# Optimization experiments

Measured on AMD Instinct MI355X. Metric: run time of the kernel, lower is better.

The kernel has to match this reference:

```python
import jax, jax.numpy as jnp
import numpy as np

EDGE_TYPES = 7
TIME_STEP = 5
STATE_DIM = 1024


def setup_inputs() -> dict:
    key = jax.random.key(0)
    ks = jax.random.split(key, 8)
    B, T, N, DF = 4, 15, 15, 25600
    S, E = STATE_DIM, EDGE_TYPES
    # weights ~ N(0, 0.01), biases zero, matching _initialization()
    return {
        "pose_features": jax.random.normal(ks[0], (B, T, N, DF), jnp.float32),
        "W_compress": jax.random.normal(ks[1], (DF, S), jnp.float32) * 0.01,
        "b_compress": jnp.zeros((S,), jnp.float32),
        "W_edge": jax.random.normal(ks[2], (E, S, S), jnp.float32) * 0.01,
        "b_edge": jnp.zeros((E, S), jnp.float32),
        "W_att": jax.random.normal(ks[3], (E, 2 * S), jnp.float32) * 0.01,
        "b_att": jnp.zeros((E,), jnp.float32),
        "W_r": jax.random.normal(ks[4], (2 * S, S), jnp.float32) * 0.01,
        "b_r": jnp.zeros((S,), jnp.float32),
        "W_z": jax.random.normal(ks[5], (2 * S, S), jnp.float32) * 0.01,
        "b_z": jnp.zeros((S,), jnp.float32),
        "W_h": jax.random.normal(ks[6], (2 * S, S), jnp.float32) * 0.01,
        "b_h": jnp.zeros((S,), jnp.float32),
    }


def reference(pose_features, W_compress, b_compress, W_edge, b_edge,
              W_att, b_att, W_r, b_r, W_z, b_z, W_h, b_h):
    B, T, N, DF = pose_features.shape
    S = W_compress.shape[1]
    E = W_edge.shape[0]
    x = pose_features.reshape(B * T, N, DF)
    prop = x @ W_compress + b_compress                      # [M, N, S]
    # attention Linear over concat(row, col) == row-part + col-part (rank-1 broadcast,
    # avoids materializing the [M, N, N, 2S] repeat/cat tensor; identical math)
    Wa_row, Wa_col = W_att[:, :S], W_att[:, S:]
    scores = None
    for _ in range(1 + TIME_STEP):
        msg = jnp.einsum('bnd,edh->benh', prop, W_edge) + b_edge[None, :, None, :]  # [M,E,N,S]
        row = jnp.einsum('bend,ed->ben', msg, Wa_row)       # [M, E, N]
        col = jnp.einsum('bend,ed->ben', msg, Wa_col)
        scores = jax.nn.sigmoid(row[..., :, None] + col[..., None, :]
                                + b_att[None, :, None, None])   # [M, E, N, N]
        merged = jnp.einsum('beij,bejd->bid', scores, msg)  # [M, N, S]
        a = jnp.concatenate([merged, prop], axis=-1)        # [M, N, 2S]
        r = jax.nn.sigmoid(a @ W_r + b_r)
        z = jax.nn.sigmoid(a @ W_z + b_z)
        h_hat = jnp.tanh(jnp.concatenate([merged, r * prop], axis=-1) @ W_h + b_h)
        prop = (1 - z) * prop + z * h_hat
    box_states = scores.transpose(0, 2, 3, 1)               # [M, N, N, E]
    action_score = ((1 - box_states[..., 0:1]) * box_states).sum(axis=2)
    action_score = action_score.reshape(B, T, N, E)
    actor_score = (1 - box_states[..., 0]).reshape(B, T, N, N)
    acty_score = jax.nn.softmax(
        (action_score * actor_score.sum(axis=-1)[..., None]).sum(axis=2)[:, :, 1:],
        axis=-1)
    return action_score, acty_score, actor_score
```

## Files before the change

kernel.cpp:

```cpp
#include <hip/hip_runtime.h>
#include <hip/hip_bf16.h>

typedef unsigned short bf16_t;
typedef __bf16 bf16x8 __attribute__((ext_vector_type(8)));
typedef float f32x4 __attribute__((ext_vector_type(4)));
typedef unsigned short ushort8_t __attribute__((ext_vector_type(8)));

__device__ __forceinline__ unsigned short f2bf(float x){
  union { __hip_bfloat16 h; unsigned short u; } c;
  c.h = __float2bfloat16(x);
  return c.u;
}
__device__ __forceinline__ float bf2f(bf16_t u){
  union { unsigned short u; __hip_bfloat16 h; } c;
  c.u = u;
  return __bfloat162float(c.h);
}
__device__ __forceinline__ ushort8_t cvt8(float4 a, float4 b){
  ushort8_t r;
  r[0]=f2bf(a.x); r[1]=f2bf(a.y); r[2]=f2bf(a.z); r[3]=f2bf(a.w);
  r[4]=f2bf(b.x); r[5]=f2bf(b.y); r[6]=f2bf(b.z); r[7]=f2bf(b.w);
  return r;
}

__device__ __forceinline__ size_t pidx(int m, int k, int KT){
  const int r = m & 127, c = (k >> 3) & 3;
  const int cs = c ^ ((r >> 1) & 3);
  return ((size_t)((m >> 7)*KT + (k >> 5)))*4096 + r*32 + cs*8 + (k & 7);
}

template<int MODE>
__global__ __launch_bounds__(512, 4)
void gemm256(const void* __restrict__ Aptr, int KTA ,
             const bf16_t* __restrict__ Bpk, int KTB,
             float* __restrict__ C, int ldc, size_t csplit,
             int M, int KchunkT)
{
  __shared__ __align__(16) bf16_t As[2][8192];
  __shared__ __align__(16) bf16_t Bs[2][4096];
  const int tid = threadIdx.x;
  const int w = tid >> 6, lane = tid & 63;
  const int wm = w >> 1, wn = w & 1;
  const int lr = lane & 15, kq = lane >> 4;
  int bcol, brow, bks;
  if (MODE == 0)      { bcol = blockIdx.x; brow = blockIdx.y; bks = blockIdx.z; }
  else if (MODE == 1) { bks = blockIdx.x;  bcol = blockIdx.y; brow = blockIdx.z; }
  else { brow = blockIdx.x & 3; bks = blockIdx.z*2 + (blockIdx.x >> 2); bcol = blockIdx.y; }
  const int gn0 = bcol*128;
  const int kt0 = bks*KchunkT, nt = KchunkT;

  const int aoff = (w & 3)*1024 + lane*8;
  const int asub = w >> 2;
  ushort8_t va0, va1, vb0;
  const bf16_t* Bg = Bpk + ((size_t)bcol*KTB + kt0)*4096 + w*512 + lane*8;
  const bf16_t* Ag = nullptr;
  const float *Af0 = nullptr, *Af1 = nullptr;
  if (MODE == 2) {
    const int r  = aoff >> 5;
    const int cs = (aoff >> 3) & 3;
    const int c  = cs ^ ((r >> 1) & 3);
    const int g0 = min(brow*256 + asub*128 + r,      M-1);
    const int g1 = min(brow*256 + asub*128 + r + 16, M-1);
    Af0 = (const float*)Aptr + (size_t)g0*KTA + (size_t)kt0*32 + c*8;
    Af1 = (const float*)Aptr + (size_t)g1*KTA + (size_t)kt0*32 + c*8;
  } else {
    Ag = (const bf16_t*)Aptr + ((size_t)(2*brow + asub)*KTA + kt0)*4096 + aoff;
  }
  bf16_t* Al = &As[0][0] + asub*4096 + aoff;
  bf16_t* Bl = &Bs[0][0] + w*512 + lane*8;

#define LDT(t) do { \
    if (MODE == 2) { \
      const float* a0 = Af0 + (size_t)(t)*32; \
      const float* a1 = Af1 + (size_t)(t)*32; \
      va0 = cvt8(*(const float4*)a0, *(const float4*)(a0 + 4)); \
      va1 = cvt8(*(const float4*)a1, *(const float4*)(a1 + 4)); \
    } else { \
      va0 = *(const ushort8_t*)(Ag + (size_t)(t)*4096); \
      va1 = *(const ushort8_t*)(Ag + (size_t)(t)*4096 + 512); \
    } \
    vb0 = *(const ushort8_t*)(Bg + (size_t)(t)*4096); \
  } while(0)
#define WRT(b) do { \
    *(ushort8_t*)(Al + (b)*8192) = va0; \
    *(ushort8_t*)(Al + (b)*8192 + 512) = va1; \
    *(ushort8_t*)(Bl + (b)*4096) = vb0; } while(0)

  LDT(0); WRT(0);
  if (nt > 1) LDT(1);
  asm volatile("s_waitcnt lgkmcnt(0)" ::: "memory");
  __builtin_amdgcn_s_barrier();
  __builtin_amdgcn_sched_barrier(0);

  const int kqs = kq ^ ((lr >> 1) & 3);
  const int abase = (wm >> 1)*4096 + ((wm & 1)*64 + lr)*32 + kqs*8;
  const int bbase = (wn*64 + lr)*32 + kqs*8;
  f32x4 acc[4][4] = {};

  for (int t = 0; t < nt; ++t) {
    const int cb = t & 1;
    const bf16_t* Ab = &As[0][0] + cb*8192 + abase;
    const bf16_t* Bb = &Bs[0][0] + cb*4096 + bbase;
    bf16x8 af[4], bfr[4];
#pragma unroll
    for (int mi = 0; mi < 4; mi++) af[mi]  = *(const bf16x8*)(Ab + mi*512);
#pragma unroll
    for (int ni = 0; ni < 4; ni++) bfr[ni] = *(const bf16x8*)(Bb + ni*512);
    if (t + 1 < nt) WRT(cb ^ 1);
    if (t + 2 < nt) LDT(t + 2);
    __builtin_amdgcn_s_setprio(1);
#pragma unroll
    for (int mi = 0; mi < 4; mi++)
#pragma unroll
      for (int ni = 0; ni < 4; ni++)
        acc[mi][ni] = __builtin_amdgcn_mfma_f32_16x16x32_bf16(af[mi], bfr[ni], acc[mi][ni], 0, 0, 0);
    __builtin_amdgcn_s_setprio(0);
    asm volatile("s_waitcnt lgkmcnt(0)" ::: "memory");
    __builtin_amdgcn_s_barrier();
    __builtin_amdgcn_sched_barrier(0);
  }
#undef LDT
#undef WRT

#pragma unroll
  for (int mi = 0; mi < 4; mi++) {
#pragma unroll
    for (int ni = 0; ni < 4; ni++) {
      const int col = gn0 + wn*64 + ni*16 + lr;
#pragma unroll
      for (int i = 0; i < 4; i++) {
        const int row = brow*256 + wm*64 + mi*16 + kq*4 + i;
        if (row < M)
          C[(size_t)bks*csplit + (size_t)row*ldc + col] = acc[mi][ni][i];
      }
    }
  }
}

__global__ void pack_b(const float* __restrict__ src, bf16_t* __restrict__ dst,
                       int srcldN, int KT, int n0t)
{
  const int ntb = blockIdx.x, kt = blockIdx.y;
  __shared__ float s[32][132];
  for (int i = threadIdx.x; i < 4096; i += 256) {
    const int kl = i >> 7, nl = i & 127;
    s[kl][nl] = src[(size_t)(kt*32 + kl)*srcldN + ntb*128 + nl];
  }
  __syncthreads();
  bf16_t* dt = dst + ((size_t)(n0t + ntb)*KT + kt)*4096;
  for (int u = threadIdx.x; u < 512; u += 256) {
    const int r = u >> 2, c = u & 3;
    const int cs = c ^ ((r >> 1) & 3);
    *(ushort4*)(dt + r*32 + cs*8) =
      make_ushort4(f2bf(s[c*8+0][r]), f2bf(s[c*8+1][r]), f2bf(s[c*8+2][r]), f2bf(s[c*8+3][r]));
    *(ushort4*)(dt + r*32 + cs*8 + 4) =
      make_ushort4(f2bf(s[c*8+4][r]), f2bf(s[c*8+5][r]), f2bf(s[c*8+6][r]), f2bf(s[c*8+7][r]));
  }
}

__global__ void reduce_compress(const float* __restrict__ part, const float* __restrict__ bias,
                                float* __restrict__ prop, bf16_t* __restrict__ Xp)
{
  const int idx = blockIdx.x*256 + threadIdx.x;
  const int m = idx >> 10, d = idx & 1023;
  float v = bias[d];
#pragma unroll
  for (int z = 0; z < 8; z++) v += part[(size_t)z*921600 + idx];
  prop[idx] = v;
  Xp[pidx(m, 1024 + d, 64)] = f2bf(v);
}

__global__ void reduce_merged(const float* __restrict__ part, const float* __restrict__ rowsumS,
                              const float* __restrict__ be,
                              bf16_t* __restrict__ Xp, bf16_t* __restrict__ Xhp)
{
  const int idx = blockIdx.x*256 + threadIdx.x;
  const int m = idx >> 10, d = idx & 1023;
  const int b = m/15, i = m - b*15;
  float v = 0.f;
#pragma unroll
  for (int z = 0; z < 8; z++) v += part[(size_t)z*921600 + idx];
#pragma unroll
  for (int e = 0; e < 7; e++)
    v += rowsumS[(b*7 + e)*15 + i] * be[e*1024 + d];
  const bf16_t o = f2bf(v);
  Xp [pidx(m, d, 64)] = o;
  Xhp[pidx(m, d, 64)] = o;
}

__global__ void reduce_rz(const float* __restrict__ part, const float* __restrict__ bias,
                          const float* __restrict__ prop, float* __restrict__ Zbuf,
                          bf16_t* __restrict__ Xhp)
{
  const int idx = blockIdx.x*256 + threadIdx.x;
  const int m = idx >> 11, c = idx & 2047;
  float v = bias[c];
#pragma unroll
  for (int z = 0; z < 4; z++) v += part[(size_t)z*1843200 + idx];
  v = 1.f / (1.f + __expf(-v));
  if (c < 1024) Xhp[pidx(m, 1024 + c, 64)] = f2bf(v * prop[(size_t)m*1024 + c]);
  else          Zbuf[(size_t)m*1024 + (c - 1024)] = v;
}

__global__ void reduce_h(const float* __restrict__ part, const float* __restrict__ bias,
                         const float* __restrict__ Zbuf, float* __restrict__ prop,
                         bf16_t* __restrict__ Xp)
{
  const int idx = blockIdx.x*256 + threadIdx.x;
  const int m = idx >> 10, d = idx & 1023;
  float v = bias[d];
#pragma unroll
  for (int z = 0; z < 4; z++) v += part[(size_t)z*921600 + idx];
  v = tanhf(v);
  const float zz = Zbuf[idx];
  const float pn = (1.f - zz)*prop[idx] + zz*v;
  prop[idx] = pn;
  Xp[pidx(m, 1024 + d, 64)] = f2bf(pn);
}

__global__ void compute_u(const float* __restrict__ We, const float* __restrict__ Wa,
                          float* __restrict__ u_row, float* __restrict__ u_col)
{
  const int w = threadIdx.x >> 6, lane = threadIdx.x & 63;
  const int idx = blockIdx.x*4 + w;
  const int e = idx >> 10, h = idx & 1023;
  const float* wep = We + ((size_t)e*1024 + h)*1024;
  const float* wr  = Wa + (size_t)e*2048;
  const float* wc  = wr + 1024;
  float ar = 0.f, ac = 0.f;
#pragma unroll
  for (int t = 0; t < 16; t++) {
    const float v = wep[lane + 64*t];
    ar += v*wr[lane + 64*t];
    ac += v*wc[lane + 64*t];
  }
  for (int off = 32; off; off >>= 1) { ar += __shfl_down(ar, off); ac += __shfl_down(ac, off); }
  if (lane == 0) { u_row[idx] = ar; u_col[idx] = ac; }
}

__global__ void crc_kernel(const float* __restrict__ be, const float* __restrict__ Wa,
                           float* __restrict__ crc)
{
  const int w = threadIdx.x >> 6, lane = threadIdx.x & 63;
  for (int idx = w; idx < 14; idx += 4) {
    const int e = idx >> 1, which = idx & 1;
    const float* bp = be + e*1024;
    const float* wp = Wa + (size_t)e*2048 + which*1024;
    float a = 0.f;
#pragma unroll
    for (int t = 0; t < 16; t++) a += bp[lane + 64*t]*wp[lane + 64*t];
    for (int off = 32; off; off >>= 1) a += __shfl_down(a, off);
    if (lane == 0) crc[which*7 + e] = a;
  }
}

__global__ void attn_kernel(const float* __restrict__ prop, const float* __restrict__ u_row,
                            const float* __restrict__ u_col, const float* __restrict__ crc,
                            const float* __restrict__ b_att, float* __restrict__ scores,
                            float* __restrict__ rowsumS)
{
  const int b = blockIdx.x, e = blockIdx.y;
  __shared__ float rowv[15], colv[15], sc_s[225];
  const int w = threadIdx.x >> 6, lane = threadIdx.x & 63;
  const float* ur = u_row + (size_t)e*1024;
  const float* uc = u_col + (size_t)e*1024;
  for (int n = w; n < 15; n += 4) {
    const float* pr = prop + (size_t)(b*15 + n)*1024;
    float ar = 0.f, ac = 0.f;
#pragma unroll
    for (int t = 0; t < 16; t++) {
      const float pv = pr[lane + 64*t];
      ar += pv*ur[lane + 64*t];
      ac += pv*uc[lane + 64*t];
    }
    for (int off = 32; off; off >>= 1) { ar += __shfl_down(ar, off); ac += __shfl_down(ac, off); }
    if (lane == 0) { rowv[n] = ar; colv[n] = ac; }
  }
  __syncthreads();
  const float base = b_att[e] + crc[e] + crc[7 + e];
  for (int idx = threadIdx.x; idx < 225; idx += 256) {
    const int i = idx/15, j = idx - i*15;
    const float s = 1.f / (1.f + __expf(-(rowv[i] + colv[j] + base)));
    scores[((size_t)(b*7 + e)*15 + i)*15 + j] = s;
    sc_s[idx] = s;
  }
  __syncthreads();
  if (threadIdx.x < 15) {
    float rs = 0.f;
#pragma unroll
    for (int j = 0; j < 15; j++) rs += sc_s[threadIdx.x*15 + j];
    rowsumS[(b*7 + e)*15 + threadIdx.x] = rs;
  }
}

__global__ __launch_bounds__(512)
void qmix_kernel(const float* __restrict__ prop, const float* __restrict__ scores,
                 bf16_t* __restrict__ Qp)
{
  const int b = blockIdx.x;
  const int d = blockIdx.y*512 + threadIdx.x;
  __shared__ float ss[1575];
  for (int idx = threadIdx.x; idx < 1575; idx += 512)
    ss[idx] = scores[(size_t)b*1575 + idx];
  float pv[15];
#pragma unroll
  for (int j = 0; j < 15; j++)
    pv[j] = prop[(size_t)(b*15 + j)*1024 + d];
  __syncthreads();
  for (int e = 0; e < 7; e++)
#pragma unroll
    for (int i = 0; i < 15; i++) {
      const float* se = ss + (e*15 + i)*15;
      float a = 0.f;
#pragma unroll
      for (int j = 0; j < 15; j++) a += se[j]*pv[j];
      Qp[pidx(b*15 + i, e*1024 + d, 224)] = f2bf(a);
    }
}

__global__ void cat2_kernel(const float* __restrict__ a, const float* __restrict__ b,
                            float* __restrict__ o)
{
  const int i = blockIdx.x*256 + threadIdx.x;
  if (i < 1024) o[i] = a[i];
  else if (i < 2048) o[i] = b[i - 1024];
}

__global__ void finalize_kernel(const float* __restrict__ scores, float* __restrict__ out)
{
  const int b = blockIdx.x;
  __shared__ float sc[1575];
  __shared__ float act[105];
  __shared__ float asum[15];
  __shared__ float t2[7];
  for (int idx = threadIdx.x; idx < 1575; idx += 256)
    sc[idx] = scores[(size_t)b*1575 + idx];
  __syncthreads();
  for (int idx = threadIdx.x; idx < 105; idx += 256) {
    const int i = idx/7, e = idx - i*7;
    float a = 0.f;
#pragma unroll
    for (int j = 0; j < 15; j++)
      a += (1.f - sc[i*15 + j]) * sc[(e*15 + i)*15 + j];
    act[idx] = a;
    out[(size_t)b*105 + idx] = a;
  }
  for (int idx = threadIdx.x; idx < 225; idx += 256) {
    const int i = idx/15, j = idx - i*15;
    out[6660 + (size_t)b*225 + idx] = 1.f - sc[i*15 + j];
  }
  if (threadIdx.x < 15) {
    const int i = threadIdx.x;
    float s = 0.f;
#pragma unroll
    for (int j = 0; j < 15; j++) s += 1.f - sc[i*15 + j];
    asum[i] = s;
  }
  __syncthreads();
  if (threadIdx.x < 7) {
    const int e = threadIdx.x;
    float t = 0.f;
#pragma unroll
    for (int i = 0; i < 15; i++) t += act[i*7 + e]*asum[i];
    t2[e] = t;
  }
  __syncthreads();
  if (threadIdx.x == 0) {
    float mx = -1e30f;
    for (int e = 1; e < 7; e++) mx = fmaxf(mx, t2[e]);
    float s = 0.f, ex[6];
    for (int e = 1; e < 7; e++) { ex[e-1] = __expf(t2[e] - mx); s += ex[e-1]; }
    for (int e = 1; e < 7; e++) out[6300 + (size_t)b*6 + (e-1)] = ex[e-1]/s;
  }
}

extern "C" void kernel_launch(void* const* d_in, const int* in_sizes, int n_in,
                              void* d_out, int out_size, void* d_ws, size_t ws_size,
                              hipStream_t stream)
{
  const float* pose = (const float*)d_in[0];
  const float* Wc   = (const float*)d_in[1];
  const float* bc   = (const float*)d_in[2];
  const float* We   = (const float*)d_in[3];
  const float* be   = (const float*)d_in[4];
  const float* Wa   = (const float*)d_in[5];
  const float* ba   = (const float*)d_in[6];
  const float* Wr   = (const float*)d_in[7];
  const float* br   = (const float*)d_in[8];
  const float* Wz   = (const float*)d_in[9];
  const float* bz   = (const float*)d_in[10];
  const float* Wh   = (const float*)d_in[11];
  const float* bh   = (const float*)d_in[12];
  float* out = (float*)d_out;

  char* p = (char*)d_ws;
  auto alloc = [&](size_t b) { char* r = p; p += (b + 255) & ~(size_t)255; return r; };
  bf16_t* Wstackp = (bf16_t*)alloc(8ull*224*8192);
  bf16_t* Wrzp    = (bf16_t*)alloc(16ull*64*8192);
  bf16_t* Whp     = (bf16_t*)alloc(8ull*64*8192);
  bf16_t* Xp      = (bf16_t*)alloc(8ull*64*8192);
  bf16_t* Xhp     = (bf16_t*)alloc(8ull*64*8192);
  float*  prop    = (float*) alloc(900ull*1024*4);
  float*  scores  = (float*) alloc(60ull*1575*4);
  float*  rowsumS = (float*) alloc(60ull*105*4);
  float*  u_row   = (float*) alloc(7168*4);
  float*  u_col   = (float*) alloc(7168*4);
  float*  crc     = (float*) alloc(64);
  float*  brzv    = (float*) alloc(2048*4);
  char* r1 = alloc(134400000ull);
  bf16_t* Wcp     = (bf16_t*)r1;
  bf16_t* Qp      = (bf16_t*)r1;
  float*  Zbuf    = (float*) (r1 + 14680064ull);
  float*  partbuf = (float*) (r1 + 52428800ull);

  compute_u<<<1792, 256, 0, stream>>>(We, Wa, u_row, u_col);
  crc_kernel<<<1, 256, 0, stream>>>(be, Wa, crc);
  cat2_kernel<<<8, 256, 0, stream>>>(br, bz, brzv);
  pack_b<<<dim3(8,800), 256, 0, stream>>>(Wc, Wcp, 1024, 800, 0);
  pack_b<<<dim3(8,224), 256, 0, stream>>>(We, Wstackp, 1024, 224, 0);
  pack_b<<<dim3(8,64),  256, 0, stream>>>(Wr, Wrzp, 1024, 64, 0);
  pack_b<<<dim3(8,64),  256, 0, stream>>>(Wz, Wrzp, 1024, 64, 8);
  pack_b<<<dim3(8,64),  256, 0, stream>>>(Wh, Whp, 1024, 64, 0);

  gemm256<2><<<dim3(8,8,4), 512, 0, stream>>>(pose, 25600, Wcp, 800,
      partbuf, 1024, 921600ull, 900, 100);
  reduce_compress<<<3600, 256, 0, stream>>>(partbuf, bc, prop, Xp);

  for (int it = 0; it < 6; it++) {
    attn_kernel<<<dim3(60,7), 256, 0, stream>>>(prop, u_row, u_col, crc, ba,
                                                scores, rowsumS);
    if (it == 5) break;
    qmix_kernel<<<dim3(60,2), 512, 0, stream>>>(prop, scores, Qp);
    gemm256<1><<<dim3(8,8,4), 512, 0, stream>>>(Qp, 224, Wstackp, 224,
        partbuf, 1024, 921600ull, 900, 28);
    reduce_merged<<<3600, 256, 0, stream>>>(partbuf, rowsumS, be, Xp, Xhp);
    gemm256<0><<<dim3(16,4,4), 512, 0, stream>>>(Xp, 64, Wrzp, 64,
        partbuf, 2048, 1843200ull, 900, 16);
    reduce_rz<<<7200, 256, 0, stream>>>(partbuf, brzv, prop, Zbuf, Xhp);
    gemm256<0><<<dim3(8,4,4), 512, 0, stream>>>(Xhp, 64, Whp, 64,
        partbuf, 1024, 921600ull, 900, 16);
    reduce_h<<<3600, 256, 0, stream>>>(partbuf, bh, Zbuf, prop, Xp);
  }

  finalize_kernel<<<60, 256, 0, stream>>>(scores, out);
}
```

Before: 778.9 us.

## Fuse attention with qmix, double split-K on GEMMs, use nontemporal partial traffic

Attention scoring and the score-weighted mixing (qmix) are merged into one kernel per batch. It stages prop as bf16 in shared memory and computes all 7 edge types per block. Every GEMM now uses twice as many split-K chunks and more blocks, and the reduce kernels sum correspondingly more partials. Partial-buffer loads and stores, plus the fp32 pose loads, become nontemporal to avoid cache pollution. The intent is better CU occupancy and fewer launches, at the cost of more partial-sum traffic and slight extra bf16 rounding of prop in qmix.

```diff
diff --git a/kernel.cpp b/kernel.cpp
--- a/kernel.cpp
+++ b/kernel.cpp
@@ -16,10 +16,10 @@
   c.u = u;
   return __bfloat162float(c.h);
 }
-__device__ __forceinline__ ushort8_t cvt8(float4 a, float4 b){
+__device__ __forceinline__ ushort8_t cvt8v(f32x4 a, f32x4 b){
   ushort8_t r;
-  r[0]=f2bf(a.x); r[1]=f2bf(a.y); r[2]=f2bf(a.z); r[3]=f2bf(a.w);
-  r[4]=f2bf(b.x); r[5]=f2bf(b.y); r[6]=f2bf(b.z); r[7]=f2bf(b.w);
+  r[0]=f2bf(a[0]); r[1]=f2bf(a[1]); r[2]=f2bf(a[2]); r[3]=f2bf(a[3]);
+  r[4]=f2bf(b[0]); r[5]=f2bf(b[1]); r[6]=f2bf(b[2]); r[7]=f2bf(b[3]);
   return r;
 }
 
@@ -43,8 +43,7 @@
   const int wm = w >> 1, wn = w & 1;
   const int lr = lane & 15, kq = lane >> 4;
   int bcol, brow, bks;
-  if (MODE == 0)      { bcol = blockIdx.x; brow = blockIdx.y; bks = blockIdx.z; }
-  else if (MODE == 1) { bks = blockIdx.x;  bcol = blockIdx.y; brow = blockIdx.z; }
+  if (MODE == 1) { bks = blockIdx.x;  bcol = blockIdx.y; brow = blockIdx.z; }
   else { brow = blockIdx.x & 3; bks = blockIdx.z*2 + (blockIdx.x >> 2); bcol = blockIdx.y; }
   const int gn0 = bcol*128;
   const int kt0 = bks*KchunkT, nt = KchunkT;
@@ -73,8 +72,10 @@
     if (MODE == 2) { \
       const float* a0 = Af0 + (size_t)(t)*32; \
       const float* a1 = Af1 + (size_t)(t)*32; \
-      va0 = cvt8(*(const float4*)a0, *(const float4*)(a0 + 4)); \
-      va1 = cvt8(*(const float4*)a1, *(const float4*)(a1 + 4)); \
+      va0 = cvt8v(__builtin_nontemporal_load((const f32x4*)a0), \
+                  __builtin_nontemporal_load((const f32x4*)(a0 + 4))); \
+      va1 = cvt8v(__builtin_nontemporal_load((const f32x4*)a1), \
+                  __builtin_nontemporal_load((const f32x4*)(a1 + 4))); \
     } else { \
       va0 = *(const ushort8_t*)(Ag + (size_t)(t)*4096); \
       va1 = *(const ushort8_t*)(Ag + (size_t)(t)*4096 + 512); \
@@ -131,7 +132,8 @@
       for (int i = 0; i < 4; i++) {
         const int row = brow*256 + wm*64 + mi*16 + kq*4 + i;
         if (row < M)
-          C[(size_t)bks*csplit + (size_t)row*ldc + col] = acc[mi][ni][i];
+          __builtin_nontemporal_store(acc[mi][ni][i],
+              &C[(size_t)bks*csplit + (size_t)row*ldc + col]);
       }
     }
   }
@@ -165,7 +167,7 @@
   const int m = idx >> 10, d = idx & 1023;
   float v = bias[d];
 #pragma unroll
-  for (int z = 0; z < 8; z++) v += part[(size_t)z*921600 + idx];
+  for (int z = 0; z < 16; z++) v += __builtin_nontemporal_load(&part[(size_t)z*921600 + idx]);
   prop[idx] = v;
   Xp[pidx(m, 1024 + d, 64)] = f2bf(v);
 }
@@ -179,7 +181,7 @@
   const int b = m/15, i = m - b*15;
   float v = 0.f;
 #pragma unroll
-  for (int z = 0; z < 8; z++) v += part[(size_t)z*921600 + idx];
+  for (int z = 0; z < 16; z++) v += __builtin_nontemporal_load(&part[(size_t)z*921600 + idx]);
 #pragma unroll
   for (int e = 0; e < 7; e++)
     v += rowsumS[(b*7 + e)*15 + i] * be[e*1024 + d];
@@ -196,7 +198,7 @@
   const int m = idx >> 11, c = idx & 2047;
   float v = bias[c];
 #pragma unroll
-  for (int z = 0; z < 4; z++) v += part[(size_t)z*1843200 + idx];
+  for (int z = 0; z < 8; z++) v += __builtin_nontemporal_load(&part[(size_t)z*1843200 + idx]);
   v = 1.f / (1.f + __expf(-v));
   if (c < 1024) Xhp[pidx(m, 1024 + c, 64)] = f2bf(v * prop[(size_t)m*1024 + c]);
   else          Zbuf[(size_t)m*1024 + (c - 1024)] = v;
@@ -210,7 +212,7 @@
   const int m = idx >> 10, d = idx & 1023;
   float v = bias[d];
 #pragma unroll
-  for (int z = 0; z < 4; z++) v += part[(size_t)z*921600 + idx];
+  for (int z = 0; z < 8; z++) v += __builtin_nontemporal_load(&part[(size_t)z*921600 + idx]);
   v = tanhf(v);
   const float zz = Zbuf[idx];
   const float pn = (1.f - zz)*prop[idx] + zz*v;
@@ -254,18 +256,28 @@
   }
 }
 
-__global__ void attn_kernel(const float* __restrict__ prop, const float* __restrict__ u_row,
-                            const float* __restrict__ u_col, const float* __restrict__ crc,
-                            const float* __restrict__ b_att, float* __restrict__ scores,
-                            float* __restrict__ rowsumS)
-{
-  const int b = blockIdx.x, e = blockIdx.y;
-  __shared__ float rowv[15], colv[15], sc_s[225];
-  const int w = threadIdx.x >> 6, lane = threadIdx.x & 63;
-  const float* ur = u_row + (size_t)e*1024;
-  const float* uc = u_col + (size_t)e*1024;
-  for (int n = w; n < 15; n += 4) {
+template<int QM>
+__global__ __launch_bounds__(512)
+void attn_qmix(const float* __restrict__ prop, const float* __restrict__ u_row,
+               const float* __restrict__ u_col, const float* __restrict__ crc,
+               const float* __restrict__ b_att, float* __restrict__ scores,
+               float* __restrict__ rowsumS, bf16_t* __restrict__ Qp)
+{
+  const int b = blockIdx.x;
+  __shared__ bf16_t ps[15*1024];
+  __shared__ float ss[1575];
+  __shared__ float rv[105], cv[105];
+  const int tid = threadIdx.x;
+  const int w = tid >> 6, lane = tid & 63;
+
+  for (int idx = tid; idx < 15360; idx += 512)
+    ps[idx] = f2bf(prop[(size_t)b*15360 + idx]);
+
+  for (int p = w; p < 105; p += 8) {
+    const int e = p/15, n = p - e*15;
     const float* pr = prop + (size_t)(b*15 + n)*1024;
+    const float* ur = u_row + (size_t)e*1024;
+    const float* uc = u_col + (size_t)e*1024;
     float ar = 0.f, ac = 0.f;
 #pragma unroll
     for (int t = 0; t < 16; t++) {
@@ -274,48 +286,43 @@
       ac += pv*uc[lane + 64*t];
     }
     for (int off = 32; off; off >>= 1) { ar += __shfl_down(ar, off); ac += __shfl_down(ac, off); }
-    if (lane == 0) { rowv[n] = ar; colv[n] = ac; }
-  }
-  __syncthreads();
-  const float base = b_att[e] + crc[e] + crc[7 + e];
-  for (int idx = threadIdx.x; idx < 225; idx += 256) {
-    const int i = idx/15, j = idx - i*15;
-    const float s = 1.f / (1.f + __expf(-(rowv[i] + colv[j] + base)));
-    scores[((size_t)(b*7 + e)*15 + i)*15 + j] = s;
-    sc_s[idx] = s;
-  }
-  __syncthreads();
-  if (threadIdx.x < 15) {
+    if (lane == 0) { rv[p] = ar; cv[p] = ac; }
+  }
+  __syncthreads();
+  for (int idx = tid; idx < 1575; idx += 512) {
+    const int e = idx/225, r = idx - e*225;
+    const int i = r/15, j = r - i*15;
+    const float s = 1.f / (1.f + __expf(-(rv[e*15+i] + cv[e*15+j] + b_att[e] + crc[e] + crc[7+e])));
+    ss[idx] = s;
+    scores[(size_t)b*1575 + idx] = s;
+  }
+  __syncthreads();
+  if (tid < 105) {
     float rs = 0.f;
 #pragma unroll
-    for (int j = 0; j < 15; j++) rs += sc_s[threadIdx.x*15 + j];
-    rowsumS[(b*7 + e)*15 + threadIdx.x] = rs;
-  }
-}
-
-__global__ __launch_bounds__(512)
-void qmix_kernel(const float* __restrict__ prop, const float* __restrict__ scores,
-                 bf16_t* __restrict__ Qp)
-{
-  const int b = blockIdx.x;
-  const int d = blockIdx.y*512 + threadIdx.x;
-  __shared__ float ss[1575];
-  for (int idx = threadIdx.x; idx < 1575; idx += 512)
-    ss[idx] = scores[(size_t)b*1575 + idx];
-  float pv[15];
-#pragma unroll
-  for (int j = 0; j < 15; j++)
-    pv[j] = prop[(size_t)(b*15 + j)*1024 + d];
-  __syncthreads();
-  for (int e = 0; e < 7; e++)
-#pragma unroll
-    for (int i = 0; i < 15; i++) {
-      const float* se = ss + (e*15 + i)*15;
-      float a = 0.f;
-#pragma unroll
-      for (int j = 0; j < 15; j++) a += se[j]*pv[j];
-      Qp[pidx(b*15 + i, e*1024 + d, 224)] = f2bf(a);
+    for (int j = 0; j < 15; j++) rs += ss[tid*15 + j];
+    rowsumS[(size_t)b*105 + tid] = rs;
+  }
+  if (QM) {
+    const int d = tid;
+    float pv[15], pw[15];
+#pragma unroll
+    for (int j = 0; j < 15; j++) {
+      pv[j] = bf2f(ps[j*1024 + d]);
+      pw[j] = bf2f(ps[j*1024 + d + 512]);
     }
+    for (int e = 0; e < 7; e++)
+#pragma unroll
+      for (int i = 0; i < 15; i++) {
+        const float* se = ss + (e*15 + i)*15;
+        float a = 0.f, c = 0.f;
+#pragma unroll
+        for (int j = 0; j < 15; j++) { a += se[j]*pv[j]; c += se[j]*pw[j]; }
+        const int m = b*15 + i;
+        Qp[pidx(m, e*1024 + d,       224)] = f2bf(a);
+        Qp[pidx(m, e*1024 + d + 512, 224)] = f2bf(c);
+      }
+  }
 }
 
 __global__ void cat2_kernel(const float* __restrict__ a, const float* __restrict__ b,
@@ -422,24 +429,27 @@
   pack_b<<<dim3(8,64),  256, 0, stream>>>(Wz, Wrzp, 1024, 64, 8);
   pack_b<<<dim3(8,64),  256, 0, stream>>>(Wh, Whp, 1024, 64, 0);
 
-  gemm256<2><<<dim3(8,8,4), 512, 0, stream>>>(pose, 25600, Wcp, 800,
-      partbuf, 1024, 921600ull, 900, 100);
+  gemm256<2><<<dim3(8,8,8), 512, 0, stream>>>(pose, 25600, Wcp, 800,
+      partbuf, 1024, 921600ull, 900, 50);
   reduce_compress<<<3600, 256, 0, stream>>>(partbuf, bc, prop, Xp);
 
   for (int it = 0; it < 6; it++) {
-    attn_kernel<<<dim3(60,7), 256, 0, stream>>>(prop, u_row, u_col, crc, ba,
-                                                scores, rowsumS);
-    if (it == 5) break;
-    qmix_kernel<<<dim3(60,2), 512, 0, stream>>>(prop, scores, Qp);
-    gemm256<1><<<dim3(8,8,4), 512, 0, stream>>>(Qp, 224, Wstackp, 224,
-        partbuf, 1024, 921600ull, 900, 28);
-    reduce_merged<<<3600, 256, 0, stream>>>(partbuf, rowsumS, be, Xp, Xhp);
-    gemm256<0><<<dim3(16,4,4), 512, 0, stream>>>(Xp, 64, Wrzp, 64,
-        partbuf, 2048, 1843200ull, 900, 16);
-    reduce_rz<<<7200, 256, 0, stream>>>(partbuf, brzv, prop, Zbuf, Xhp);
-    gemm256<0><<<dim3(8,4,4), 512, 0, stream>>>(Xhp, 64, Whp, 64,
-        partbuf, 1024, 921600ull, 900, 16);
-    reduce_h<<<3600, 256, 0, stream>>>(partbuf, bh, Zbuf, prop, Xp);
+    if (it < 5) {
+      attn_qmix<1><<<60, 512, 0, stream>>>(prop, u_row, u_col, crc, ba,
+                                           scores, rowsumS, Qp);
+      gemm256<1><<<dim3(16,8,4), 512, 0, stream>>>(Qp, 224, Wstackp, 224,
+          partbuf, 1024, 921600ull, 900, 14);
+      reduce_merged<<<3600, 256, 0, stream>>>(partbuf, rowsumS, be, Xp, Xhp);
+      gemm256<1><<<dim3(8,16,4), 512, 0, stream>>>(Xp, 64, Wrzp, 64,
+          partbuf, 2048, 1843200ull, 900, 8);
+      reduce_rz<<<7200, 256, 0, stream>>>(partbuf, brzv, prop, Zbuf, Xhp);
+      gemm256<1><<<dim3(8,8,4), 512, 0, stream>>>(Xhp, 64, Whp, 64,
+          partbuf, 1024, 921600ull, 900, 8);
+      reduce_h<<<3600, 256, 0, stream>>>(partbuf, bh, Zbuf, prop, Xp);
+    } else {
+      attn_qmix<0><<<60, 512, 0, stream>>>(prop, u_row, u_col, crc, ba,
+                                           scores, rowsumS, Qp);
+    }
   }
 
   finalize_kernel<<<60, 256, 0, stream>>>(scores, out);
```

After: 1.047 ms. 1.34x slower.
